# Kernel optimization log

Measured on AMD Instinct MI355X. Metric: run time of the kernel, lower is better.

## Reference

```python
import jax, jax.numpy as jnp
import numpy as np

D = 768
NH = 8
HD = D // NH
DFF = 2048
EPS = 1e-5


def _layer_norm(x, g, b):
    mu = jnp.mean(x, axis=-1, keepdims=True)
    var = jnp.mean(jnp.square(x - mu), axis=-1, keepdims=True)
    return (x - mu) * jax.lax.rsqrt(var + EPS) * g + b


def setup_inputs() -> dict:
    key = jax.random.key(0)
    ks = jax.random.split(key, 16)
    B, L = 2, 2048
    s = 0.02
    return {
        "x": jax.random.normal(ks[0], (B, L, D), jnp.float32),
        "attn_bias": jax.random.normal(ks[1], (B, L, L), jnp.float32),
        "in_proj_w": jax.random.normal(ks[2], (3 * D, D), jnp.float32) * s,
        "in_proj_b": jnp.zeros((3 * D,), jnp.float32),
        "out_w": jax.random.normal(ks[3], (D, D), jnp.float32) * s,
        "out_b": jnp.zeros((D,), jnp.float32),
        "W1": jax.random.normal(ks[4], (DFF, D), jnp.float32) * s,
        "b1": jnp.zeros((DFF,), jnp.float32),
        "W2": jax.random.normal(ks[5], (D, DFF), jnp.float32) * s,
        "b2": jnp.zeros((D,), jnp.float32),
        "g1": jnp.ones((D,), jnp.float32),
        "be1": jnp.zeros((D,), jnp.float32),
        "g2": jnp.ones((D,), jnp.float32),
        "be2": jnp.zeros((D,), jnp.float32),
    }


def reference(x, attn_bias, in_proj_w, in_proj_b, out_w, out_b,
              W1, b1, W2, b2, g1, be1, g2, be2):
    B, L, _ = x.shape
    # fused qkv projection (torch nn.MultiheadAttention in_proj)
    qkv = x @ in_proj_w.T + in_proj_b          # [B, L, 3D]
    q, k, v = jnp.split(qkv, 3, axis=-1)
    q = q.reshape(B, L, NH, HD).transpose(0, 2, 1, 3)  # [B, nH, L, hd]
    k = k.reshape(B, L, NH, HD).transpose(0, 2, 1, 3)
    v = v.reshape(B, L, NH, HD).transpose(0, 2, 1, 3)
    scale = 1.0 / jnp.sqrt(jnp.asarray(HD, x.dtype))
    scores = jnp.einsum("bhqd,bhkd->bhqk", q * scale, k)
    scores = scores + attn_bias[:, None, :, :]         # broadcast over heads == expand
    attn = jax.nn.softmax(scores, axis=-1)
    ctx = jnp.einsum("bhqk,bhkd->bhqd", attn, v)       # [B, nH, L, hd]
    ctx = ctx.transpose(0, 2, 1, 3).reshape(B, L, D)
    attn_out = ctx @ out_w.T + out_b
    x = _layer_norm(x + attn_out, g1, be1)
    h = jax.nn.gelu(x @ W1.T + b1, approximate=False)  # torch default GELU = erf
    ff = h @ W2.T + b2
    return _layer_norm(x + ff, g2, be2)
```

## Files before the change

### kernel.cpp

```cpp
#include <hip/hip_runtime.h>
#include <hip/hip_bf16.h>
#include <math.h>

typedef __bf16 bf16;
typedef __attribute__((ext_vector_type(8))) __bf16 bf16x8;
typedef __attribute__((ext_vector_type(4))) __bf16 bf16x4;
typedef __attribute__((ext_vector_type(4))) float f32x4;

#define LOG2E 1.4426950408889634f

__device__ __forceinline__ void gload16(const bf16* g, bf16* l) {
  __builtin_amdgcn_global_load_lds(
      (const __attribute__((address_space(1))) void*)g,
      (__attribute__((address_space(3))) void*)l, 16, 0, 0);
}

struct CastSegs { const float* src[6]; bf16* dst[6]; };

__global__ void fused_cast_kernel(CastSegs segs) {
  const int e0 = 786432, e1 = 1228800, e2 = 1376256, e3 = 1769472, e4 = 2162688, e5 = 4259840;
  int i = blockIdx.x * blockDim.x + threadIdx.x;
  int stride = gridDim.x * blockDim.x;
  for (; i < e5; i += stride) {
    int s = 0, base = 0;
    if (i >= e0) { s = 1; base = e0; }
    if (i >= e1) { s = 2; base = e1; }
    if (i >= e2) { s = 3; base = e2; }
    if (i >= e3) { s = 4; base = e3; }
    if (i >= e4) { s = 5; base = e4; }
    float4 v = ((const float4*)segs.src[s])[i - base];
    bf16x4 o = { (bf16)v.x, (bf16)v.y, (bf16)v.z, (bf16)v.w };
    ((bf16x4*)segs.dst[s])[i - base] = o;
  }
}

__launch_bounds__(256)
__global__ void vtrans_kernel(const bf16* __restrict__ qkv, bf16* __restrict__ vt) {
  __shared__ bf16 T[96][72];
  const int t = threadIdx.x;
  const int tk0 = blockIdx.x * 64;
  const int h = blockIdx.y, b = blockIdx.z;
  const bf16* vp = qkv + ((size_t)b * 2048 + tk0) * 2304 + 1536 + h * 96;
  const int row = t >> 2;
  const int cb = (t & 3) * 24;
#pragma unroll
  for (int i = 0; i < 3; i++) {
    bf16x8 v = *(const bf16x8*)(vp + (size_t)row * 2304 + cb + i * 8);
#pragma unroll
    for (int j = 0; j < 8; j++) T[cb + i * 8 + j][row] = v[j];
  }
  __syncthreads();
  bf16* op = vt + (size_t)((b * 8 + h) * 96) * 2048 + tk0;
#pragma unroll
  for (int i = 0; i < 3; i++) {
    int hd = (t >> 3) + i * 32;
    int tk = (t & 7) * 8;
    *(bf16x8*)(op + (size_t)hd * 2048 + tk) = *(const bf16x8*)&T[hd][tk];
  }
}

template<int MODE>
__launch_bounds__(256)
__global__ void gemm_kernel(const bf16* __restrict__ A, const bf16* __restrict__ W,
                            const float* __restrict__ bias, const float* __restrict__ res,
                            void* __restrict__ out, int K, int O) {
  __shared__ bf16 As[128 * 64];
  __shared__ bf16 Bs[128 * 64];
  const int t    = threadIdx.x;
  const int lane = t & 63;
  const int wave = t >> 6;
  const int wr = (wave >> 1) * 64;
  const int wc = (wave & 1) * 64;
  const int n0 = blockIdx.y * 128;
  const int o0 = blockIdx.x * 128;

  f32x4 zero = {0.f, 0.f, 0.f, 0.f};
  f32x4 acc[4][4];
#pragma unroll
  for (int m = 0; m < 4; m++)
#pragma unroll
    for (int n = 0; n < 4; n++) acc[m][n] = zero;

  const int fr  = lane & 15;
  const int fg8 = (lane >> 4) * 8;

  for (int k0 = 0; k0 < K; k0 += 64) {
    __syncthreads();
#pragma unroll
    for (int c = 0; c < 4; c++) {
      int f = c * 256 + t;
      int row = f >> 3;
      int col = (f & 7) * 8;
      gload16(&A[(size_t)(n0 + row) * K + k0 + col], &As[f * 8]);
      gload16(&W[(size_t)(o0 + row) * K + k0 + col], &Bs[f * 8]);
    }
    __syncthreads();
#pragma unroll
    for (int kf = 0; kf < 2; kf++) {
      bf16x8 a[4], b[4];
#pragma unroll
      for (int m = 0; m < 4; m++) a[m] = *(const bf16x8*)&As[(wr + m * 16 + fr) * 64 + kf * 32 + fg8];
#pragma unroll
      for (int n = 0; n < 4; n++) b[n] = *(const bf16x8*)&Bs[(wc + n * 16 + fr) * 64 + kf * 32 + fg8];
#pragma unroll
      for (int m = 0; m < 4; m++)
#pragma unroll
        for (int n = 0; n < 4; n++)
          acc[m][n] = __builtin_amdgcn_mfma_f32_16x16x32_bf16(a[m], b[n], acc[m][n], 0, 0, 0);
    }
  }

  const int fg4 = (lane >> 4) * 4;
#pragma unroll
  for (int m = 0; m < 4; m++) {
#pragma unroll
    for (int n = 0; n < 4; n++) {
      int col = o0 + wc + n * 16 + fr;
      float bv = bias[col];
#pragma unroll
      for (int r = 0; r < 4; r++) {
        int row = n0 + wr + m * 16 + fg4 + r;
        float v = acc[m][n][r] + bv;
        if constexpr (MODE == 2) {
          v = 0.5f * v * (1.0f + erff(v * 0.70710678118654752f));
          ((bf16*)out)[(size_t)row * O + col] = (bf16)v;
        } else {
          ((bf16*)out)[(size_t)row * O + col] = (bf16)v;
        }
      }
    }
  }
}

__launch_bounds__(256)
__global__ void gemm64_kernel(const bf16* __restrict__ A, const bf16* __restrict__ W,
                              const float* __restrict__ bias, const float* __restrict__ res,
                              float* __restrict__ out, int K, int O) {
  __shared__ bf16 As[64 * 64];
  __shared__ bf16 Bs[64 * 64];
  const int t    = threadIdx.x;
  const int lane = t & 63;
  const int wave = t >> 6;
  const int wr = (wave >> 1) * 32;
  const int wc = (wave & 1) * 32;
  const int n0 = blockIdx.y * 64;
  const int o0 = blockIdx.x * 64;

  f32x4 zero = {0.f, 0.f, 0.f, 0.f};
  f32x4 acc[2][2];
#pragma unroll
  for (int m = 0; m < 2; m++)
#pragma unroll
    for (int n = 0; n < 2; n++) acc[m][n] = zero;

  const int fr  = lane & 15;
  const int fg8 = (lane >> 4) * 8;

  for (int k0 = 0; k0 < K; k0 += 64) {
    __syncthreads();
#pragma unroll
    for (int c = 0; c < 2; c++) {
      int f = c * 256 + t;
      int row = f >> 3;
      int col = (f & 7) * 8;
      gload16(&A[(size_t)(n0 + row) * K + k0 + col], &As[f * 8]);
      gload16(&W[(size_t)(o0 + row) * K + k0 + col], &Bs[f * 8]);
    }
    __syncthreads();
#pragma unroll
    for (int kf = 0; kf < 2; kf++) {
      bf16x8 a[2], b[2];
#pragma unroll
      for (int m = 0; m < 2; m++) a[m] = *(const bf16x8*)&As[(wr + m * 16 + fr) * 64 + kf * 32 + fg8];
#pragma unroll
      for (int n = 0; n < 2; n++) b[n] = *(const bf16x8*)&Bs[(wc + n * 16 + fr) * 64 + kf * 32 + fg8];
#pragma unroll
      for (int m = 0; m < 2; m++)
#pragma unroll
        for (int n = 0; n < 2; n++)
          acc[m][n] = __builtin_amdgcn_mfma_f32_16x16x32_bf16(a[m], b[n], acc[m][n], 0, 0, 0);
    }
  }

  const int fg4 = (lane >> 4) * 4;
#pragma unroll
  for (int m = 0; m < 2; m++) {
#pragma unroll
    for (int n = 0; n < 2; n++) {
      int col = o0 + wc + n * 16 + fr;
      float bv = bias[col];
#pragma unroll
      for (int r = 0; r < 4; r++) {
        int row = n0 + wr + m * 16 + fg4 + r;
        float v = acc[m][n][r] + bv + res[(size_t)row * O + col];
        out[(size_t)row * O + col] = v;
      }
    }
  }
}

__launch_bounds__(512, 4)
__global__ void attn_kernel(const bf16* __restrict__ qkv, const bf16* __restrict__ vt,
                            const bf16* __restrict__ biasb, float* __restrict__ opart,
                            float* __restrict__ ml) {
  __shared__ bf16 Ks[2][64][104];
  __shared__ bf16 Vs[2][96][72];
  __shared__ bf16 Pl[8][16][72];
  const int t    = threadIdx.x;
  const int lane = t & 63;
  const int wave = t >> 6;
  const int qb = blockIdx.x, h = blockIdx.y;
  const int half = blockIdx.z & 1, b = blockIdx.z >> 1;
  const int kvstart = half * 1024;
  const int q0 = qb * 128 + wave * 16;
  const int fq = lane & 15;
  const int g  = lane >> 4;
  const size_t base = (size_t)b * 2048 * 2304;

  bf16x8 qf[3];
  {
    const bf16* qp = qkv + base + (size_t)(q0 + fq) * 2304 + h * 96;
#pragma unroll
    for (int f = 0; f < 3; f++) qf[f] = *(const bf16x8*)(qp + f * 32 + g * 8);
  }

  const int kr1 = t >> 3, kc1 = (t & 7) * 8;
  const int kr2 = t >> 2, kc2 = 64 + (t & 3) * 8;
  const int vr2 = 64 + (t >> 3);
  const bf16* kbase = qkv + base + (size_t)kvstart * 2304 + 768 + h * 96;
  const bf16* vbase = vt + (size_t)((b * 8 + h) * 96) * 2048 + kvstart;

  bf16x8 kreg0, kreg1, vreg0, vreg1;
  const bool lo = (t < 256);

  kreg0 = *(const bf16x8*)(kbase + (size_t)kr1 * 2304 + kc1);
  vreg0 = *(const bf16x8*)(vbase + (size_t)kr1 * 2048 + kc1);
  if (lo) {
    kreg1 = *(const bf16x8*)(kbase + (size_t)kr2 * 2304 + kc2);
    vreg1 = *(const bf16x8*)(vbase + (size_t)vr2 * 2048 + kc1);
  }

  float m_run = -1e30f, l_run = 0.f;
  f32x4 zero = {0.f, 0.f, 0.f, 0.f};
  f32x4 o_acc[6];
#pragma unroll
  for (int i = 0; i < 6; i++) o_acc[i] = zero;

  const float scale = 0.10206207261596575f;
  const bf16* bp = biasb + ((size_t)b * 2048 + q0 + fq) * 2048 + kvstart;

  int cur = 0;
  for (int kv0 = 0; kv0 < 1024; kv0 += 64) {
    *(bf16x8*)&Ks[cur][kr1][kc1] = kreg0;
    *(bf16x8*)&Vs[cur][kr1][kc1] = vreg0;
    if (lo) {
      *(bf16x8*)&Ks[cur][kr2][kc2] = kreg1;
      *(bf16x8*)&Vs[cur][vr2][kc1] = vreg1;
    }
    __syncthreads();

    if (kv0 + 64 < 1024) {
      int nx = kv0 + 64;
      kreg0 = *(const bf16x8*)(kbase + (size_t)(nx + kr1) * 2304 + kc1);
      vreg0 = *(const bf16x8*)(vbase + (size_t)kr1 * 2048 + nx + kc1);
      if (lo) {
        kreg1 = *(const bf16x8*)(kbase + (size_t)(nx + kr2) * 2304 + kc2);
        vreg1 = *(const bf16x8*)(vbase + (size_t)vr2 * 2048 + nx + kc1);
      }
    }
    __builtin_amdgcn_sched_barrier(0);

    bf16x4 bb[4];
#pragma unroll
    for (int kvt = 0; kvt < 4; kvt++)
      bb[kvt] = *(const bf16x4*)(bp + kv0 + kvt * 16 + g * 4);

    f32x4 s[4];
#pragma unroll
    for (int kvt = 0; kvt < 4; kvt++) {
      s[kvt] = zero;
#pragma unroll
      for (int f = 0; f < 3; f++) {
        bf16x8 kfr = *(const bf16x8*)&Ks[cur][kvt * 16 + fq][f * 32 + g * 8];
        s[kvt] = __builtin_amdgcn_mfma_f32_16x16x32_bf16(kfr, qf[f], s[kvt], 0, 0, 0);
      }
    }

    float p[4][4];
    float vmax = -1e30f;
#pragma unroll
    for (int kvt = 0; kvt < 4; kvt++) {
#pragma unroll
      for (int r = 0; r < 4; r++) {
        float sv = s[kvt][r] * scale + (float)bb[kvt][r];
        p[kvt][r] = sv;
        vmax = fmaxf(vmax, sv);
      }
    }
    vmax = fmaxf(vmax, __shfl_xor(vmax, 16));
    vmax = fmaxf(vmax, __shfl_xor(vmax, 32));
    if (!__all(vmax <= m_run + 8.0f)) {
      float m_new = fmaxf(m_run, vmax);
      float corr = exp2f((m_run - m_new) * LOG2E);
      l_run *= corr;
#pragma unroll
      for (int i = 0; i < 6; i++)
#pragma unroll
        for (int r = 0; r < 4; r++) o_acc[i][r] *= corr;
      m_run = m_new;
    }
    float rsum = 0.f;
#pragma unroll
    for (int kvt = 0; kvt < 4; kvt++) {
      bf16x4 pb;
#pragma unroll
      for (int r = 0; r < 4; r++) {
        float pv = exp2f((p[kvt][r] - m_run) * LOG2E);
        rsum += pv;
        pb[r] = (bf16)pv;
      }
      *(bf16x4*)&Pl[wave][fq][kvt * 16 + g * 4] = pb;
    }
    rsum += __shfl_xor(rsum, 16);
    rsum += __shfl_xor(rsum, 32);
    l_run += rsum;

#pragma unroll
    for (int kf = 0; kf < 2; kf++) {
      bf16x8 pfrag = *(const bf16x8*)&Pl[wave][fq][kf * 32 + g * 8];
#pragma unroll
      for (int ht = 0; ht < 6; ht++) {
        bf16x8 vfrag = *(const bf16x8*)&Vs[cur][ht * 16 + fq][kf * 32 + g * 8];
        o_acc[ht] = __builtin_amdgcn_mfma_f32_16x16x32_bf16(vfrag, pfrag, o_acc[ht], 0, 0, 0);
      }
    }
    cur ^= 1;
  }

  float* op = opart + (size_t)half * (16 * 2048 * 96) + ((size_t)(b * 8 + h) * 2048 + q0 + fq) * 96;
  float* mlp = ml + ((size_t)half * 32768 + (size_t)(b * 8 + h) * 2048 + q0 + fq) * 2;
#pragma unroll
  for (int ht = 0; ht < 6; ht++)
    *(f32x4*)&op[ht * 16 + g * 4] = o_acc[ht];
  if (g == 0) { mlp[0] = m_run; mlp[1] = l_run; }
}

__launch_bounds__(256)
__global__ void attn_combine_kernel(const float* __restrict__ opart, const float* __restrict__ ml,
                                    bf16* __restrict__ ctx) {
  int idx = blockIdx.x * blockDim.x + threadIdx.x;
  if (idx >= 786432) return;
  int e = idx * 4;
  int bh = e / (2048 * 96);
  int rem = e - bh * (2048 * 96);
  int q = rem / 96;
  int hd = rem - q * 96;
  const float* op0 = opart;
  const float* op1 = opart + (size_t)16 * 2048 * 96;
  float4 o1 = *(const float4*)&op0[e];
  float4 o2 = *(const float4*)&op1[e];
  const float* ml0 = ml + (size_t)(bh * 2048 + q) * 2;
  const float* ml1 = ml0 + (size_t)32768 * 2;
  float m1 = ml0[0], l1 = ml0[1];
  float m2 = ml1[0], l2 = ml1[1];
  float M = fmaxf(m1, m2);
  float w1 = exp2f((m1 - M) * LOG2E);
  float w2 = exp2f((m2 - M) * LOG2E);
  float inv = 1.0f / (l1 * w1 + l2 * w2);
  int b = bh >> 3, h = bh & 7;
  bf16x4 o;
  o[0] = (bf16)((o1.x * w1 + o2.x * w2) * inv);
  o[1] = (bf16)((o1.y * w1 + o2.y * w2) * inv);
  o[2] = (bf16)((o1.z * w1 + o2.z * w2) * inv);
  o[3] = (bf16)((o1.w * w1 + o2.w * w2) * inv);
  *(bf16x4*)&ctx[((size_t)b * 2048 + q) * 768 + h * 96 + hd] = o;
}

__launch_bounds__(256)
__global__ void ln_kernel(const float* in, const float* __restrict__ gamma,
                          const float* __restrict__ beta, float* outf, bf16* outb) {
  const int row = blockIdx.x;
  const int t = threadIdx.x;
  const float* rp = in + (size_t)row * 768;
  float v[3];
#pragma unroll
  for (int i = 0; i < 3; i++) v[i] = rp[t + 256 * i];
  float s = v[0] + v[1] + v[2];
  float ss = v[0] * v[0] + v[1] * v[1] + v[2] * v[2];
#pragma unroll
  for (int off = 1; off < 64; off <<= 1) {
    s += __shfl_xor(s, off);
    ss += __shfl_xor(ss, off);
  }
  __shared__ float red[8];
  if ((t & 63) == 0) { red[(t >> 6) * 2] = s; red[(t >> 6) * 2 + 1] = ss; }
  __syncthreads();
  s = red[0] + red[2] + red[4] + red[6];
  ss = red[1] + red[3] + red[5] + red[7];
  float mu = s * (1.0f / 768.0f);
  float var = ss * (1.0f / 768.0f) - mu * mu;
  float rs = rsqrtf(var + 1e-5f);
#pragma unroll
  for (int i = 0; i < 3; i++) {
    int col = t + 256 * i;
    float y = (v[i] - mu) * rs * gamma[col] + beta[col];
    outf[(size_t)row * 768 + col] = y;
    if (outb) outb[(size_t)row * 768 + col] = (bf16)y;
  }
}

extern "C" void kernel_launch(void* const* d_in, const int* in_sizes, int n_in,
                              void* d_out, int out_size, void* d_ws, size_t ws_size,
                              hipStream_t stream) {
  (void)in_sizes; (void)n_in; (void)out_size; (void)ws_size;
  const float* x     = (const float*)d_in[0];
  const float* ab    = (const float*)d_in[1];
  const float* w_qkv = (const float*)d_in[2];
  const float* b_qkv = (const float*)d_in[3];
  const float* w_out = (const float*)d_in[4];
  const float* b_out = (const float*)d_in[5];
  const float* W1    = (const float*)d_in[6];
  const float* b1    = (const float*)d_in[7];
  const float* W2    = (const float*)d_in[8];
  const float* b2    = (const float*)d_in[9];
  const float* g1    = (const float*)d_in[10];
  const float* be1   = (const float*)d_in[11];
  const float* g2    = (const float*)d_in[12];
  const float* be2   = (const float*)d_in[13];
  float* outf = (float*)d_out;

  char* p = (char*)d_ws;
  bf16* xb    = (bf16*)p;  p += (size_t)4096 * 768 * 2;
  bf16* qkv   = (bf16*)p;  p += (size_t)4096 * 2304 * 2;
  bf16* ctx   = (bf16*)p;  p += (size_t)4096 * 768 * 2;
  float* x1f  = (float*)p; p += (size_t)4096 * 768 * 4;
  bf16* x1b   = (bf16*)p;  p += (size_t)4096 * 768 * 2;
  bf16* hbuf  = (bf16*)p;  p += (size_t)4096 * 2048 * 2;
  bf16* wqkvb = (bf16*)p;  p += (size_t)2304 * 768 * 2;
  bf16* woutb = (bf16*)p;  p += (size_t)768 * 768 * 2;
  bf16* w1b   = (bf16*)p;  p += (size_t)2048 * 768 * 2;
  bf16* w2b   = (bf16*)p;  p += (size_t)768 * 2048 * 2;
  float* opart = (float*)p; p += (size_t)2 * 16 * 2048 * 96 * 4;
  float* mlb   = (float*)p; p += (size_t)2 * 32768 * 2 * 4;
  bf16* vtb   = (bf16*)x1f;
  bf16* biasb = hbuf;

  CastSegs segs;
  segs.src[0] = x;     segs.dst[0] = xb;
  segs.src[1] = w_qkv; segs.dst[1] = wqkvb;
  segs.src[2] = w_out; segs.dst[2] = woutb;
  segs.src[3] = W1;    segs.dst[3] = w1b;
  segs.src[4] = W2;    segs.dst[4] = w2b;
  segs.src[5] = ab;    segs.dst[5] = biasb;
  fused_cast_kernel<<<2048, 256, 0, stream>>>(segs);

  gemm_kernel<0><<<dim3(18, 32), 256, 0, stream>>>(xb, wqkvb, b_qkv, nullptr, qkv, 768, 2304);
  vtrans_kernel<<<dim3(32, 8, 2), 256, 0, stream>>>(qkv, vtb);
  attn_kernel<<<dim3(16, 8, 4), 512, 0, stream>>>(qkv, vtb, biasb, opart, mlb);
  attn_combine_kernel<<<3072, 256, 0, stream>>>(opart, mlb, ctx);
  gemm64_kernel<<<dim3(12, 64), 256, 0, stream>>>(ctx, woutb, b_out, x, outf, 768, 768);
  ln_kernel<<<4096, 256, 0, stream>>>(outf, g1, be1, x1f, x1b);
  gemm_kernel<2><<<dim3(16, 32), 256, 0, stream>>>(x1b, w1b, b1, nullptr, hbuf, 768, 2048);
  gemm64_kernel<<<dim3(12, 64), 256, 0, stream>>>(hbuf, w2b, b2, x1f, outf, 2048, 768);
  ln_kernel<<<4096, 256, 0, stream>>>(outf, g2, be2, outf, nullptr);
}
```

Measured before the change: 217.8 us.

## Fuse V transpose into QKV GEMM, read fp32 bias directly, widen output GEMM tiles

The QKV GEMM epilogue now writes the V columns straight into the transposed vt layout, which removes the separate vtrans kernel. The attention-bias cast to bf16 is dropped, so the attention kernel reads fp32 bias directly and fuses the scale with an fma. The old 64x64 residual GEMM becomes a 128x64-tile kernel with a 4x2 MFMA layout per wave, halving the grid. The trade-off is that the attention kernel now reads twice as many bias bytes, and the vt stores are 8-byte scattered writes.

After: 216.5 us. Within noise of the previous version (-0.6%).

```diff
diff --git a/kernel.cpp b/kernel.cpp
--- a/kernel.cpp
+++ b/kernel.cpp
@@ -15,54 +15,28 @@
       (__attribute__((address_space(3))) void*)l, 16, 0, 0);
 }
 
-struct CastSegs { const float* src[6]; bf16* dst[6]; };
+struct CastSegs { const float* src[5]; bf16* dst[5]; };
 
 __global__ void fused_cast_kernel(CastSegs segs) {
-  const int e0 = 786432, e1 = 1228800, e2 = 1376256, e3 = 1769472, e4 = 2162688, e5 = 4259840;
+  const int e0 = 786432, e1 = 1228800, e2 = 1376256, e3 = 1769472, e4 = 2162688;
   int i = blockIdx.x * blockDim.x + threadIdx.x;
   int stride = gridDim.x * blockDim.x;
-  for (; i < e5; i += stride) {
+  for (; i < e4; i += stride) {
     int s = 0, base = 0;
     if (i >= e0) { s = 1; base = e0; }
     if (i >= e1) { s = 2; base = e1; }
     if (i >= e2) { s = 3; base = e2; }
     if (i >= e3) { s = 4; base = e3; }
-    if (i >= e4) { s = 5; base = e4; }
     float4 v = ((const float4*)segs.src[s])[i - base];
     bf16x4 o = { (bf16)v.x, (bf16)v.y, (bf16)v.z, (bf16)v.w };
     ((bf16x4*)segs.dst[s])[i - base] = o;
   }
 }
 
-__launch_bounds__(256)
-__global__ void vtrans_kernel(const bf16* __restrict__ qkv, bf16* __restrict__ vt) {
-  __shared__ bf16 T[96][72];
-  const int t = threadIdx.x;
-  const int tk0 = blockIdx.x * 64;
-  const int h = blockIdx.y, b = blockIdx.z;
-  const bf16* vp = qkv + ((size_t)b * 2048 + tk0) * 2304 + 1536 + h * 96;
-  const int row = t >> 2;
-  const int cb = (t & 3) * 24;
-#pragma unroll
-  for (int i = 0; i < 3; i++) {
-    bf16x8 v = *(const bf16x8*)(vp + (size_t)row * 2304 + cb + i * 8);
-#pragma unroll
-    for (int j = 0; j < 8; j++) T[cb + i * 8 + j][row] = v[j];
-  }
-  __syncthreads();
-  bf16* op = vt + (size_t)((b * 8 + h) * 96) * 2048 + tk0;
-#pragma unroll
-  for (int i = 0; i < 3; i++) {
-    int hd = (t >> 3) + i * 32;
-    int tk = (t & 7) * 8;
-    *(bf16x8*)(op + (size_t)hd * 2048 + tk) = *(const bf16x8*)&T[hd][tk];
-  }
-}
-
 template<int MODE>
 __launch_bounds__(256)
 __global__ void gemm_kernel(const bf16* __restrict__ A, const bf16* __restrict__ W,
-                            const float* __restrict__ bias, const float* __restrict__ res,
+                            const float* __restrict__ bias, bf16* __restrict__ vt,
                             void* __restrict__ out, int K, int O) {
   __shared__ bf16 As[128 * 64];
   __shared__ bf16 Bs[128 * 64];
@@ -117,6 +91,21 @@
     for (int n = 0; n < 4; n++) {
       int col = o0 + wc + n * 16 + fr;
       float bv = bias[col];
+      if constexpr (MODE == 3) {
+        if (col >= 1536) {
+          int c = col - 1536;
+          int h = c / 96;
+          int hd = c - h * 96;
+          int row0 = n0 + wr + m * 16 + fg4;
+          int b = row0 >> 11;
+          int token = row0 & 2047;
+          bf16x4 ov;
+#pragma unroll
+          for (int r = 0; r < 4; r++) ov[r] = (bf16)(acc[m][n][r] + bv);
+          *(bf16x4*)&vt[((size_t)((b * 8 + h) * 96 + hd)) * 2048 + token] = ov;
+          continue;
+        }
+      }
 #pragma unroll
       for (int r = 0; r < 4; r++) {
         int row = n0 + wr + m * 16 + fg4 + r;
@@ -133,51 +122,56 @@
 }
 
 __launch_bounds__(256)
-__global__ void gemm64_kernel(const bf16* __restrict__ A, const bf16* __restrict__ W,
-                              const float* __restrict__ bias, const float* __restrict__ res,
-                              float* __restrict__ out, int K, int O) {
-  __shared__ bf16 As[64 * 64];
+__global__ void gemmW_kernel(const bf16* __restrict__ A, const bf16* __restrict__ W,
+                             const float* __restrict__ bias, const float* __restrict__ res,
+                             float* __restrict__ out, int K, int O) {
+  __shared__ bf16 As[128 * 64];
   __shared__ bf16 Bs[64 * 64];
   const int t    = threadIdx.x;
   const int lane = t & 63;
   const int wave = t >> 6;
-  const int wr = (wave >> 1) * 32;
-  const int wc = (wave & 1) * 32;
-  const int n0 = blockIdx.y * 64;
+  const int wr = wave * 32;
+  const int n0 = blockIdx.y * 128;
   const int o0 = blockIdx.x * 64;
 
   f32x4 zero = {0.f, 0.f, 0.f, 0.f};
-  f32x4 acc[2][2];
+  f32x4 acc[2][4];
 #pragma unroll
   for (int m = 0; m < 2; m++)
 #pragma unroll
-    for (int n = 0; n < 2; n++) acc[m][n] = zero;
+    for (int n = 0; n < 4; n++) acc[m][n] = zero;
 
   const int fr  = lane & 15;
   const int fg8 = (lane >> 4) * 8;
 
   for (int k0 = 0; k0 < K; k0 += 64) {
     __syncthreads();
+#pragma unroll
+    for (int c = 0; c < 4; c++) {
+      int f = c * 256 + t;
+      int row = f >> 3;
+      int col = (f & 7) * 8;
+      gload16(&A[(size_t)(n0 + row) * K + k0 + col], &As[f * 8]);
+    }
 #pragma unroll
     for (int c = 0; c < 2; c++) {
       int f = c * 256 + t;
       int row = f >> 3;
       int col = (f & 7) * 8;
-      gload16(&A[(size_t)(n0 + row) * K + k0 + col], &As[f * 8]);
       gload16(&W[(size_t)(o0 + row) * K + k0 + col], &Bs[f * 8]);
     }
     __syncthreads();
 #pragma unroll
     for (int kf = 0; kf < 2; kf++) {
-      bf16x8 a[2], b[2];
+      bf16x8 a[2], b[4];
 #pragma unroll
       for (int m = 0; m < 2; m++) a[m] = *(const bf16x8*)&As[(wr + m * 16 + fr) * 64 + kf * 32 + fg8];
 #pragma unroll
-      for (int n = 0; n < 2; n++) b[n] = *(const bf16x8*)&Bs[(wc + n * 16 + fr) * 64 + kf * 32 + fg8];
+      for (int n = 0; n < 4; n++) b[n] = *(const bf16x8*)&Bs[(n * 16 + fr) * 64 + kf * 32 + fg8];
 #pragma unroll
       for (int m = 0; m < 2; m++)
 #pragma unroll
-        for (int n = 0; n < 2; n++)
+        for (int n = 0; n < 4; n++)
           acc[m][n] = __builtin_amdgcn_mfma_f32_16x16x32_bf16(a[m], b[n], acc[m][n], 0, 0, 0);
     }
   }
@@ -186,8 +180,8 @@
 #pragma unroll
   for (int m = 0; m < 2; m++) {
 #pragma unroll
-    for (int n = 0; n < 2; n++) {
-      int col = o0 + wc + n * 16 + fr;
+    for (int n = 0; n < 4; n++) {
+      int col = o0 + n * 16 + fr;
       float bv = bias[col];
 #pragma unroll
       for (int r = 0; r < 4; r++) {
@@ -201,7 +195,7 @@
 
 __launch_bounds__(512, 4)
 __global__ void attn_kernel(const bf16* __restrict__ qkv, const bf16* __restrict__ vt,
-                            const bf16* __restrict__ biasb, float* __restrict__ opart,
+                            const float* __restrict__ bias, float* __restrict__ opart,
                             float* __restrict__ ml) {
   __shared__ bf16 Ks[2][64][104];
   __shared__ bf16 Vs[2][96][72];
@@ -247,7 +241,7 @@
   for (int i = 0; i < 6; i++) o_acc[i] = zero;
 
   const float scale = 0.10206207261596575f;
-  const bf16* bp = biasb + ((size_t)b * 2048 + q0 + fq) * 2048 + kvstart;
+  const float* bp = bias + ((size_t)b * 2048 + q0 + fq) * 2048 + kvstart;
 
   int cur = 0;
   for (int kv0 = 0; kv0 < 1024; kv0 += 64) {
@@ -270,10 +264,10 @@
     }
     __builtin_amdgcn_sched_barrier(0);
 
-    bf16x4 bb[4];
+    float4 bf[4];
 #pragma unroll
     for (int kvt = 0; kvt < 4; kvt++)
-      bb[kvt] = *(const bf16x4*)(bp + kv0 + kvt * 16 + g * 4);
+      bf[kvt] = *(const float4*)(bp + kv0 + kvt * 16 + g * 4);
 
     f32x4 s[4];
 #pragma unroll
@@ -292,7 +286,7 @@
     for (int kvt = 0; kvt < 4; kvt++) {
 #pragma unroll
       for (int r = 0; r < 4; r++) {
-        float sv = s[kvt][r] * scale + (float)bb[kvt][r];
+        float sv = fmaf(s[kvt][r], scale, (&bf[kvt].x)[r]);
         p[kvt][r] = sv;
         vmax = fmaxf(vmax, sv);
       }
@@ -443,7 +437,6 @@
   float* opart = (float*)p; p += (size_t)2 * 16 * 2048 * 96 * 4;
   float* mlb   = (float*)p; p += (size_t)2 * 32768 * 2 * 4;
   bf16* vtb   = (bf16*)x1f;
-  bf16* biasb = hbuf;
 
   CastSegs segs;
   segs.src[0] = x;     segs.dst[0] = xb;
@@ -451,16 +444,14 @@
   segs.src[2] = w_out; segs.dst[2] = woutb;
   segs.src[3] = W1;    segs.dst[3] = w1b;
   segs.src[4] = W2;    segs.dst[4] = w2b;
-  segs.src[5] = ab;    segs.dst[5] = biasb;
   fused_cast_kernel<<<2048, 256, 0, stream>>>(segs);
 
-  gemm_kernel<0><<<dim3(18, 32), 256, 0, stream>>>(xb, wqkvb, b_qkv, nullptr, qkv, 768, 2304);
-  vtrans_kernel<<<dim3(32, 8, 2), 256, 0, stream>>>(qkv, vtb);
-  attn_kernel<<<dim3(16, 8, 4), 512, 0, stream>>>(qkv, vtb, biasb, opart, mlb);
+  gemm_kernel<3><<<dim3(18, 32), 256, 0, stream>>>(xb, wqkvb, b_qkv, vtb, qkv, 768, 2304);
+  attn_kernel<<<dim3(16, 8, 4), 512, 0, stream>>>(qkv, vtb, ab, opart, mlb);
   attn_combine_kernel<<<3072, 256, 0, stream>>>(opart, mlb, ctx);
-  gemm64_kernel<<<dim3(12, 64), 256, 0, stream>>>(ctx, woutb, b_out, x, outf, 768, 768);
+  gemmW_kernel<<<dim3(12, 32), 256, 0, stream>>>(ctx, woutb, b_out, x, outf, 768, 768);
   ln_kernel<<<4096, 256, 0, stream>>>(outf, g1, be1, x1f, x1b);
   gemm_kernel<2><<<dim3(16, 32), 256, 0, stream>>>(x1b, w1b, b1, nullptr, hbuf, 768, 2048);
-  gemm64_kernel<<<dim3(12, 64), 256, 0, stream>>>(hbuf, w2b, b2, x1f, outf, 2048, 768);
+  gemmW_kernel<<<dim3(12, 32), 256, 0, stream>>>(hbuf, w2b, b2, x1f, outf, 2048, 768);
   ln_kernel<<<4096, 256, 0, stream>>>(outf, g2, be2, outf, nullptr);
 }
```
